# Kernel tuning notes

Hardware: AMD Instinct MI355X
Metric: run time of the kernel (lower is better)

## Reference

```python
import jax, jax.numpy as jnp
import numpy as np

N = 50000      # nodes
E = 800000     # edges
F_IN = 128     # input_channels
H = 128        # hidden_channels
OUT = 10       # output_channels
G = 64         # graphs in batch


def setup_inputs() -> dict:
    key = jax.random.key(0)
    ks = jax.random.split(key, 16)
    s = 0.05
    inp = {
        "x": jax.random.normal(ks[0], (N, F_IN), jnp.float32),
        "edge_index": jax.random.randint(ks[1], (2, E), 0, N, jnp.int64 if jax.config.jax_enable_x64 else jnp.int32),
        "batch": jnp.sort(jax.random.randint(ks[2], (N,), 0, G, jnp.int32)),
        "conv1_w": jax.random.normal(ks[3], (F_IN, H), jnp.float32) * s,
        "conv1_b": jnp.zeros((H,), jnp.float32),
        "conv2_w": jax.random.normal(ks[4], (H, H), jnp.float32) * s,
        "conv2_b": jnp.zeros((H,), jnp.float32),
        "conv3_w": jax.random.normal(ks[5], (H, H), jnp.float32) * s,
        "conv3_b": jnp.zeros((H,), jnp.float32),
        "fc1_w": jax.random.normal(ks[6], (H, 8 * H), jnp.float32) * s,
        "fc1_b": jnp.zeros((8 * H,), jnp.float32),
        "fc2_w": jax.random.normal(ks[7], (8 * H, 4 * H), jnp.float32) * s,
        "fc2_b": jnp.zeros((4 * H,), jnp.float32),
        "fc3_w": jax.random.normal(ks[8], (4 * H, 2 * H), jnp.float32) * s,
        "fc3_b": jnp.zeros((2 * H,), jnp.float32),
        "fc4_w": jax.random.normal(ks[9], (2 * H, H), jnp.float32) * s,
        "fc4_b": jnp.zeros((H,), jnp.float32),
        "fc5_w": jax.random.normal(ks[10], (H, OUT), jnp.float32) * s,
        "fc5_b": jnp.zeros((OUT,), jnp.float32),
    }
    return inp


def _gcn_conv(x, w, b, src, dst, norm, n_nodes):
    # GCNConv: out = D^{-1/2} (A + I) D^{-1/2} X W + b   (self-loops already in src/dst)
    xw = x @ w                                        # [N, H]
    msg = xw[src] * norm[:, None]                     # gather + scale, [E+N, H]
    return jax.ops.segment_sum(msg, dst, num_segments=n_nodes) + b


def reference(x, edge_index, batch,
              conv1_w, conv1_b, conv2_w, conv2_b, conv3_w, conv3_b,
              fc1_w, fc1_b, fc2_w, fc2_b, fc3_w, fc3_b,
              fc4_w, fc4_b, fc5_w, fc5_b):
    n = x.shape[0]
    loop = jnp.arange(n, dtype=edge_index.dtype)
    src = jnp.concatenate([edge_index[0], loop])      # add self-loops
    dst = jnp.concatenate([edge_index[1], loop])
    deg = jax.ops.segment_sum(jnp.ones_like(dst, dtype=x.dtype), dst, num_segments=n)
    dinv = jnp.where(deg > 0, jax.lax.rsqrt(deg), 0.0)
    norm = dinv[src] * dinv[dst]                      # symmetric normalization per edge

    h = jax.nn.relu(_gcn_conv(x, conv1_w, conv1_b, src, dst, norm, n))
    h = jax.nn.relu(_gcn_conv(h, conv2_w, conv2_b, src, dst, norm, n))
    h = _gcn_conv(h, conv3_w, conv3_b, src, dst, norm, n)

    # global mean pool over graphs
    sums = jax.ops.segment_sum(h, batch, num_segments=G)
    cnt = jax.ops.segment_sum(jnp.ones((n,), x.dtype), batch, num_segments=G)
    f = sums / jnp.maximum(cnt, 1.0)[:, None]         # [G, H]

    y = jax.nn.relu(f @ fc1_w + fc1_b)
    y = jax.nn.relu(y @ fc2_w + fc2_b)
    y = jax.nn.relu(y @ fc3_w + fc3_b)
    y = jax.nn.relu(y @ fc4_w + fc4_b)
    # dropout p=0.5 is identity in eval mode
    y = y @ fc5_w + fc5_b                             # [G, OUT]
    return (f, y)
```

## Files before the change

### kernel.cpp

```cpp
#include <hip/hip_runtime.h>
#include <stdint.h>

#define N_NODES 50000
#define N_EDGES 800000
#define FEAT    128
#define NGRAPH  64

#define E_BLKS    3125
#define GEMM_BLKS 6250
#define GR_BLKS   (GEMM_BLKS + E_BLKS)

typedef __attribute__((ext_vector_type(8))) short short8;
typedef __attribute__((ext_vector_type(4))) float floatx4;

static __device__ __forceinline__ ushort f2bf(float f) {
  uint32_t x = __float_as_uint(f);
  x += 0x7FFF + ((x >> 16) & 1);
  return (ushort)(x >> 16);
}
static __device__ __forceinline__ float bfLo(uint32_t u) {
  return __uint_as_float(u << 16);
}
static __device__ __forceinline__ float bfHi(uint32_t u) {
  return __uint_as_float(u & 0xFFFF0000u);
}

static __device__ __forceinline__ void cvt4T(const float* __restrict__ in,
                                             ushort* __restrict__ outT, int i) {
  float4 v = ((const float4*)in)[i];
  int k = (4 * i) >> 7;
  int n = (4 * i) & 127;
  outT[(size_t)(n + 0) * FEAT + k] = f2bf(v.x);
  outT[(size_t)(n + 1) * FEAT + k] = f2bf(v.y);
  outT[(size_t)(n + 2) * FEAT + k] = f2bf(v.z);
  outT[(size_t)(n + 3) * FEAT + k] = f2bf(v.w);
}

__global__ __launch_bounds__(256) void wcvt(const float* __restrict__ w0,
                                            const float* __restrict__ w1,
                                            ushort* __restrict__ wbT) {
  int i = blockIdx.x * 256 + threadIdx.x;
  if (i < 4096) cvt4T(w0, wbT, i);
  else cvt4T(w1, wbT + FEAT * FEAT, i - 4096);
}

static __device__ __forceinline__ void gemm_body_f32a(int wave, int lane,
                                                      const float* __restrict__ X,
                                                      const ushort* __restrict__ WT,
                                                      ushort* __restrict__ XW) {
  int mt = wave >> 3;
  int nt = wave & 7;
  int m0 = mt * 16, n0 = nt * 16;
  int r = lane & 15, quad = lane >> 4;
  floatx4 acc = {0.f, 0.f, 0.f, 0.f};
  const float* xrow = X + (size_t)(m0 + r) * FEAT;
  const ushort* wrow = WT + (size_t)(n0 + r) * FEAT;
#pragma unroll
  for (int kb = 0; kb < 4; ++kb) {
    int k0 = kb * 32 + quad * 8;
    float4 f0 = *(const float4*)(xrow + k0);
    float4 f1 = *(const float4*)(xrow + k0 + 4);
    short8 a;
    a[0] = (short)f2bf(f0.x); a[1] = (short)f2bf(f0.y);
    a[2] = (short)f2bf(f0.z); a[3] = (short)f2bf(f0.w);
    a[4] = (short)f2bf(f1.x); a[5] = (short)f2bf(f1.y);
    a[6] = (short)f2bf(f1.z); a[7] = (short)f2bf(f1.w);
    short8 b = *(const short8*)(wrow + k0);
    acc = __builtin_amdgcn_mfma_f32_16x16x32_bf16(a, b, acc, 0, 0, 0);
  }
#pragma unroll
  for (int reg = 0; reg < 4; ++reg) {
    int row = quad * 4 + reg;
    XW[(size_t)(m0 + row) * FEAT + n0 + r] = f2bf(acc[reg]);
  }
}

__global__ __launch_bounds__(256) void gemm_rank(const float* __restrict__ x,
                                                 const ushort* __restrict__ wbT,
                                                 ushort* __restrict__ msl,
                                                 const int* __restrict__ dst,
                                                 int* __restrict__ cnt,
                                                 int* __restrict__ rank) {
  int b = blockIdx.x, t = threadIdx.x;
  int third = b / 3;
  int rem = b - third * 3;
  if (rem < 2) {
    int gb = third * 2 + rem;
    gemm_body_f32a(gb * 4 + (t >> 6), t & 63, x, wbT, msl);
  } else {
    int e = third * 256 + t;
    rank[e] = atomicAdd(&cnt[dst[e]], 1);
  }
}

__global__ __launch_bounds__(256) void dinv_scan1(const int* __restrict__ cnt,
                                                  const int* __restrict__ batch,
                                                  float* __restrict__ dinv,
                                                  float* __restrict__ cnt_g,
                                                  int* __restrict__ ptr,
                                                  int* __restrict__ bsums) {
  __shared__ int tmp[256];
  __shared__ int bins[NGRAPH];
  if (threadIdx.x < NGRAPH) bins[threadIdx.x] = 0;
  int i = blockIdx.x * 256 + threadIdx.x;
  int v = (i < N_NODES) ? cnt[i] : 0;
  tmp[threadIdx.x] = v;
  __syncthreads();
  for (int off = 1; off < 256; off <<= 1) {
    int t = (threadIdx.x >= off) ? tmp[threadIdx.x - off] : 0;
    __syncthreads();
    tmp[threadIdx.x] += t;
    __syncthreads();
  }
  if (i < N_NODES) ptr[i] = tmp[threadIdx.x] - v;
  if (threadIdx.x == 255) bsums[blockIdx.x] = tmp[255];
  if (i < N_NODES) {
    dinv[i] = rsqrtf((float)v + 1.0f);
    atomicAdd(&bins[batch[i]], 1);
  }
  __syncthreads();
  if (threadIdx.x < NGRAPH && bins[threadIdx.x] > 0)
    atomicAdd(&cnt_g[threadIdx.x], (float)bins[threadIdx.x]);
}

__global__ __launch_bounds__(256) void scan2(int* __restrict__ bsums, int nb) {
  __shared__ int tmp[256];
  int v = (threadIdx.x < nb) ? bsums[threadIdx.x] : 0;
  tmp[threadIdx.x] = v;
  __syncthreads();
  for (int off = 1; off < 256; off <<= 1) {
    int t = (threadIdx.x >= off) ? tmp[threadIdx.x - off] : 0;
    __syncthreads();
    tmp[threadIdx.x] += t;
    __syncthreads();
  }
  if (threadIdx.x < nb) bsums[threadIdx.x] = tmp[threadIdx.x] - v;
}

__global__ __launch_bounds__(256) void scan3(int* __restrict__ ptr,
                                             const int* __restrict__ bsums) {
  int i = blockIdx.x * 256 + threadIdx.x;
  if (i < N_NODES) ptr[i] += bsums[blockIdx.x];
}

__global__ __launch_bounds__(256) void fill_csr(const int* __restrict__ src,
                                                const int* __restrict__ dst,
                                                const int* __restrict__ rank,
                                                const int* __restrict__ ptr,
                                                const float* __restrict__ dinv,
                                                int2* __restrict__ edges) {
  int e = blockIdx.x * 256 + threadIdx.x;
  if (e >= N_EDGES) return;
  int s = src[e];
  edges[ptr[dst[e]] + rank[e]] = make_int2(s, __float_as_int(dinv[s]));
}

__global__ __launch_bounds__(256) void gemm128(const ushort* __restrict__ X,
                                               const ushort* __restrict__ WT,
                                               ushort* __restrict__ XW) {
  int wave = (blockIdx.x * 256 + threadIdx.x) >> 6;
  int lane = threadIdx.x & 63;
  int mt = wave >> 3;
  int nt = wave & 7;
  int m0 = mt * 16, n0 = nt * 16;
  int r = lane & 15, quad = lane >> 4;
  floatx4 acc = {0.f, 0.f, 0.f, 0.f};
  const ushort* xrow = X + (size_t)(m0 + r) * FEAT;
  const ushort* wrow = WT + (size_t)(n0 + r) * FEAT;
#pragma unroll
  for (int kb = 0; kb < 4; ++kb) {
    int k0 = kb * 32 + quad * 8;
    short8 a = *(const short8*)(xrow + k0);
    short8 b = *(const short8*)(wrow + k0);
    acc = __builtin_amdgcn_mfma_f32_16x16x32_bf16(a, b, acc, 0, 0, 0);
  }
#pragma unroll
  for (int reg = 0; reg < 4; ++reg) {
    int row = quad * 4 + reg;
    XW[(size_t)(m0 + row) * FEAT + n0 + r] = f2bf(acc[reg]);
  }
}

template <int MODE>
__global__ __launch_bounds__(256) void agg_kernel(const ushort* __restrict__ msg,
                                                  const float* __restrict__ dinv,
                                                  const int* __restrict__ ptr,
                                                  const int* __restrict__ cnt,
                                                  const int2* __restrict__ edges,
                                                  const float* __restrict__ bias,
                                                  void* __restrict__ outp) {
  int wave = (blockIdx.x * 256 + threadIdx.x) >> 6;
  int lane = threadIdx.x & 63;
  if (wave >= N_NODES) return;
  int v = wave;
  float di = dinv[v];
  const uint32_t* m32 = (const uint32_t*)msg;
  uint32_t su = m32[(size_t)v * 64 + lane];
  float ax0 = di * bfLo(su), ay0 = di * bfHi(su);
  float ax1 = 0.f, ay1 = 0.f, ax2 = 0.f, ay2 = 0.f, ax3 = 0.f, ay3 = 0.f;
  int start = ptr[v];
  int n = cnt[v];
  int i = 0;
  if ((start & 1) && n > 0) {
    int2 e = edges[start];
    uint32_t u = m32[(size_t)e.x * 64 + lane];
    float nrm = __int_as_float(e.y);
    ax0 = fmaf(nrm, bfLo(u), ax0);
    ay0 = fmaf(nrm, bfHi(u), ay0);
    i = 1;
  }
  for (; i + 8 <= n; i += 8) {
    const int4* ep = (const int4*)(edges + start + i);
    int4 q0 = ep[0], q1 = ep[1], q2 = ep[2], q3 = ep[3];
    uint32_t u0 = m32[(size_t)q0.x * 64 + lane];
    uint32_t u1 = m32[(size_t)q0.z * 64 + lane];
    uint32_t u2 = m32[(size_t)q1.x * 64 + lane];
    uint32_t u3 = m32[(size_t)q1.z * 64 + lane];
    uint32_t u4 = m32[(size_t)q2.x * 64 + lane];
    uint32_t u5 = m32[(size_t)q2.z * 64 + lane];
    uint32_t u6 = m32[(size_t)q3.x * 64 + lane];
    uint32_t u7 = m32[(size_t)q3.z * 64 + lane];
    float n0 = __int_as_float(q0.y), n1 = __int_as_float(q0.w);
    float n2 = __int_as_float(q1.y), n3 = __int_as_float(q1.w);
    float n4 = __int_as_float(q2.y), n5 = __int_as_float(q2.w);
    float n6 = __int_as_float(q3.y), n7 = __int_as_float(q3.w);
    ax0 = fmaf(n0, bfLo(u0), ax0); ay0 = fmaf(n0, bfHi(u0), ay0);
    ax1 = fmaf(n1, bfLo(u1), ax1); ay1 = fmaf(n1, bfHi(u1), ay1);
    ax2 = fmaf(n2, bfLo(u2), ax2); ay2 = fmaf(n2, bfHi(u2), ay2);
    ax3 = fmaf(n3, bfLo(u3), ax3); ay3 = fmaf(n3, bfHi(u3), ay3);
    ax0 = fmaf(n4, bfLo(u4), ax0); ay0 = fmaf(n4, bfHi(u4), ay0);
    ax1 = fmaf(n5, bfLo(u5), ax1); ay1 = fmaf(n5, bfHi(u5), ay1);
    ax2 = fmaf(n6, bfLo(u6), ax2); ay2 = fmaf(n6, bfHi(u6), ay2);
    ax3 = fmaf(n7, bfLo(u7), ax3); ay3 = fmaf(n7, bfHi(u7), ay3);
  }
  for (; i < n; ++i) {
    int2 e = edges[start + i];
    float nrm = __int_as_float(e.y);
    uint32_t u = m32[(size_t)e.x * 64 + lane];
    ax0 = fmaf(nrm, bfLo(u), ax0);
    ay0 = fmaf(nrm, bfHi(u), ay0);
  }
  float ax = (ax0 + ax1) + (ax2 + ax3);
  float ay = (ay0 + ay1) + (ay2 + ay3);
  if (MODE == 2) {
    ((float2*)outp)[(size_t)v * 64 + lane] = make_float2(ax * di, ay * di);
  } else {
    ax = fmaf(ax, di, bias[2 * lane]);
    ay = fmaf(ay, di, bias[2 * lane + 1]);
    ax = fmaxf(ax, 0.f);
    ay = fmaxf(ay, 0.f);
    ushort2 h2;
    h2.x = f2bf(ax);
    h2.y = f2bf(ay);
    ((ushort2*)outp)[(size_t)v * 64 + lane] = h2;
  }
}

__global__ __launch_bounds__(256) void pool_sum(const float* __restrict__ a3,
                                                const int* __restrict__ batch,
                                                float* __restrict__ P) {
  int wave = blockIdx.x * 4 + (threadIdx.x >> 6);
  int lane = threadIdx.x & 63;
  int v0 = wave * 16;
  if (v0 >= N_NODES) return;
  int vend = v0 + 16;
  if (vend > N_NODES) vend = N_NODES;
  const float2* a2 = (const float2*)a3;
  float ax = 0.f, ay = 0.f;
  int g = batch[v0];
  for (int v = v0; v < vend; ++v) {
    int gv = batch[v];
    if (gv != g) {
      atomicAdd(&P[(size_t)g * FEAT + 2 * lane], ax);
      atomicAdd(&P[(size_t)g * FEAT + 2 * lane + 1], ay);
      ax = 0.f; ay = 0.f; g = gv;
    }
    float2 t = a2[(size_t)v * 64 + lane];
    ax += t.x;
    ay += t.y;
  }
  atomicAdd(&P[(size_t)g * FEAT + 2 * lane], ax);
  atomicAdd(&P[(size_t)g * FEAT + 2 * lane + 1], ay);
}

template <int K, int C, int KSLICE, int RELU_IN, int DIVC, int NSPLIT>
__global__ __launch_bounds__(256) void fc_layer(const float* __restrict__ IN,
                                                const float* __restrict__ W,
                                                const float* __restrict__ Bs,
                                                const float* __restrict__ cntg,
                                                float* __restrict__ OUT) {
  constexpr int CB = (C + 63) / 64;
  int lane = threadIdx.x & 63;
  int gq = threadIdx.x >> 6;
  int bid = blockIdx.x;
  int kp = bid % NSPLIT;
  int rest = bid / NSPLIT;
  int cg = rest % CB;
  int g = (rest / CB) * 4 + gq;
  int c = cg * 64 + lane;
  if (c >= C) return;
  int k0 = kp * KSLICE;
  const float* wp = W + (size_t)k0 * C + c;
  const float* in = IN + (size_t)g * K + k0;
  float cf = 1.f;
  if (DIVC) cf = fmaxf(cntg[g], 1.f);
  float a0 = 0.f, a1 = 0.f, a2 = 0.f, a3 = 0.f;
  float a4 = 0.f, a5 = 0.f, a6 = 0.f, a7 = 0.f;
#pragma unroll 2
  for (int k = 0; k < KSLICE; k += 8) {
    float i0 = in[k + 0], i1 = in[k + 1], i2 = in[k + 2], i3 = in[k + 3];
    float i4 = in[k + 4], i5 = in[k + 5], i6 = in[k + 6], i7 = in[k + 7];
    if (RELU_IN) {
      i0 = fmaxf(i0, 0.f); i1 = fmaxf(i1, 0.f);
      i2 = fmaxf(i2, 0.f); i3 = fmaxf(i3, 0.f);
      i4 = fmaxf(i4, 0.f); i5 = fmaxf(i5, 0.f);
      i6 = fmaxf(i6, 0.f); i7 = fmaxf(i7, 0.f);
    }
    if (DIVC) {
      i0 /= cf; i1 /= cf; i2 /= cf; i3 /= cf;
      i4 /= cf; i5 /= cf; i6 /= cf; i7 /= cf;
    }
    a0 = fmaf(i0, wp[(size_t)(k + 0) * C], a0);
    a1 = fmaf(i1, wp[(size_t)(k + 1) * C], a1);
    a2 = fmaf(i2, wp[(size_t)(k + 2) * C], a2);
    a3 = fmaf(i3, wp[(size_t)(k + 3) * C], a3);
    a4 = fmaf(i4, wp[(size_t)(k + 4) * C], a4);
    a5 = fmaf(i5, wp[(size_t)(k + 5) * C], a5);
    a6 = fmaf(i6, wp[(size_t)(k + 6) * C], a6);
    a7 = fmaf(i7, wp[(size_t)(k + 7) * C], a7);
  }
  float s = ((a0 + a1) + (a2 + a3)) + ((a4 + a5) + (a6 + a7));
  if (NSPLIT == 1) {
    OUT[(size_t)g * C + c] = s + Bs[c];
  } else {
    atomicAdd(&OUT[(size_t)g * C + c], s + (kp == 0 ? Bs[c] : 0.f));
  }
}

extern "C" void kernel_launch(void* const* d_in, const int* in_sizes, int n_in,
                              void* d_out, int out_size, void* d_ws, size_t ws_size,
                              hipStream_t stream) {
  const float* x         = (const float*)d_in[0];
  const int*   ei        = (const int*)d_in[1];
  const int*   batch     = (const int*)d_in[2];
  const float* conv_w[3] = {(const float*)d_in[3], (const float*)d_in[5], (const float*)d_in[7]};
  const float* conv_b[3] = {(const float*)d_in[4], (const float*)d_in[6], (const float*)d_in[8]};
  const float* fc_w[5]   = {(const float*)d_in[9],  (const float*)d_in[11],
                            (const float*)d_in[13], (const float*)d_in[15],
                            (const float*)d_in[17]};
  const float* fc_b[5]   = {(const float*)d_in[10], (const float*)d_in[12],
                            (const float*)d_in[14], (const float*)d_in[16],
                            (const float*)d_in[18]};
  const int* e_src = ei;
  const int* e_dst = ei + N_EDGES;
  float* out_f = (float*)d_out;
  float* out_y = (float*)d_out + NGRAPH * FEAT;

  char* p = (char*)d_ws;
  auto carve = [&](size_t bytes) {
    char* r = p;
    p += (bytes + 255) & ~(size_t)255;
    return r;
  };
  int*    cnt_i   = (int*)carve(N_NODES * 4);
  float*  dinv    = (float*)carve(N_NODES * 4);
  int*    csr_ptr = (int*)carve(N_NODES * 4);
  int*    bsums   = (int*)carve(256 * 4);
  int2*   edges   = (int2*)carve((size_t)N_EDGES * 8);
  ushort* wbT     = (ushort*)carve((size_t)2 * FEAT * FEAT * 2);
  ushort* hbuf    = (ushort*)carve((size_t)N_NODES * FEAT * 2);
  float*  f_sum   = (float*)carve(NGRAPH * FEAT * 4);
  float*  cnt_g   = (float*)carve(NGRAPH * 4);
  float*  Y1      = (float*)carve(NGRAPH * 1024 * 4);
  float*  Y2      = (float*)carve(NGRAPH * 512 * 4);
  float*  Y3      = (float*)carve(NGRAPH * 256 * 4);
  float*  Y4      = (float*)carve(NGRAPH * 128 * 4);
  char*   region  = carve((size_t)N_NODES * FEAT * 4);
  int*    rank    = (int*)region;
  ushort* msl     = (ushort*)(region + (size_t)N_EDGES * 4);
  float*  a3      = (float*)region;

  const int BLK_N = (N_NODES + 255) / 256;

  hipMemsetAsync(cnt_i, 0, N_NODES * 4, stream);
  hipMemsetAsync(f_sum, 0, NGRAPH * FEAT * 4 + 256, stream);
  hipMemsetAsync(Y2, 0, NGRAPH * (512 + 256 + 128) * 4, stream);

  wcvt<<<32, 256, 0, stream>>>(conv_w[0], conv_w[1], wbT);

  gemm_rank<<<GR_BLKS, 256, 0, stream>>>(x, wbT, msl, e_dst, cnt_i, rank);

  dinv_scan1<<<BLK_N, 256, 0, stream>>>(cnt_i, batch, dinv, cnt_g, csr_ptr, bsums);
  scan2<<<1, 256, 0, stream>>>(bsums, BLK_N);
  scan3<<<BLK_N, 256, 0, stream>>>(csr_ptr, bsums);

  fill_csr<<<E_BLKS, 256, 0, stream>>>(e_src, e_dst, rank, csr_ptr, dinv, edges);

  const int AGG_BLKS  = (N_NODES + 3) / 4;
  const int POOL_BLKS = (N_NODES / 16 + 3) / 4 + 1;

  agg_kernel<0><<<AGG_BLKS, 256, 0, stream>>>(msl, dinv, csr_ptr, cnt_i, edges,
                                              conv_b[0], hbuf);
  gemm128<<<GEMM_BLKS, 256, 0, stream>>>(hbuf, wbT + FEAT * FEAT, msl);
  agg_kernel<0><<<AGG_BLKS, 256, 0, stream>>>(msl, dinv, csr_ptr, cnt_i, edges,
                                              conv_b[1], hbuf);
  agg_kernel<2><<<AGG_BLKS, 256, 0, stream>>>(hbuf, dinv, csr_ptr, cnt_i, edges,
                                              nullptr, a3);
  pool_sum<<<POOL_BLKS, 256, 0, stream>>>(a3, batch, f_sum);

  fc_layer< 128, 128, 128, 0, 1, 1><<< 32, 256, 0, stream>>>(f_sum, conv_w[2], conv_b[2], cnt_g, out_f);
  fc_layer< 128,1024, 128, 0, 0, 1><<<256, 256, 0, stream>>>(out_f, fc_w[0], fc_b[0], nullptr, Y1);
  fc_layer<1024, 512, 256, 1, 0, 4><<<512, 256, 0, stream>>>(Y1, fc_w[1], fc_b[1], nullptr, Y2);
  fc_layer< 512, 256, 128, 1, 0, 4><<<256, 256, 0, stream>>>(Y2, fc_w[2], fc_b[2], nullptr, Y3);
  fc_layer< 256, 128,  32, 1, 0, 8><<<256, 256, 0, stream>>>(Y3, fc_w[3], fc_b[3], nullptr, Y4);
  fc_layer< 128,  10, 128, 1, 0, 1><<< 16, 256, 0, stream>>>(Y4, fc_w[4], fc_b[4], nullptr, out_y);
}
```

Measured before the change: 375.0 us.

## Fuse layer-1 aggregation with layer-2 GEMM and use row-strip GEMM

Layer-1 aggregation now writes its ReLU'd bf16 features for 16 nodes into shared memory, and the same block runs the layer-2 MFMA GEMM on them. This removes the separate gemm128 launch and the round trip of the hidden buffer through global memory. The first GEMM in gemm_rank also changes so each wave computes a full 16-row strip across all 8 column tiles, converting X rows once instead of eight times. This shifts the block ratio with the rank atomics to 1:4. The fused kernel uses 512-thread blocks and a block-wide barrier, which may lower occupancy for the gather-heavy aggregation phase.

```diff
diff --git a/kernel.cpp b/kernel.cpp
--- a/kernel.cpp
+++ b/kernel.cpp
@@ -6,9 +6,9 @@
 #define FEAT    128
 #define NGRAPH  64
 
-#define E_BLKS    3125
-#define GEMM_BLKS 6250
-#define GR_BLKS   (GEMM_BLKS + E_BLKS)
+#define E_BLKS      3125
+#define GSTRIP_BLKS 782
+#define GR_BLKS     (GSTRIP_BLKS + E_BLKS)
 
 typedef __attribute__((ext_vector_type(8))) short short8;
 typedef __attribute__((ext_vector_type(4))) float floatx4;
@@ -44,17 +44,15 @@
   else cvt4T(w1, wbT + FEAT * FEAT, i - 4096);
 }
 
-static __device__ __forceinline__ void gemm_body_f32a(int wave, int lane,
-                                                      const float* __restrict__ X,
-                                                      const ushort* __restrict__ WT,
-                                                      ushort* __restrict__ XW) {
-  int mt = wave >> 3;
-  int nt = wave & 7;
-  int m0 = mt * 16, n0 = nt * 16;
+static __device__ __forceinline__ void gemm_strip_f32a(int strip, int lane,
+                                                       const float* __restrict__ X,
+                                                       const ushort* __restrict__ WT,
+                                                       ushort* __restrict__ XW) {
+  if (strip >= N_NODES / 16) return;
+  int m0 = strip * 16;
   int r = lane & 15, quad = lane >> 4;
-  floatx4 acc = {0.f, 0.f, 0.f, 0.f};
   const float* xrow = X + (size_t)(m0 + r) * FEAT;
-  const ushort* wrow = WT + (size_t)(n0 + r) * FEAT;
+  short8 afr[4];
 #pragma unroll
   for (int kb = 0; kb < 4; ++kb) {
     int k0 = kb * 32 + quad * 8;
@@ -65,13 +63,21 @@
     a[2] = (short)f2bf(f0.z); a[3] = (short)f2bf(f0.w);
     a[4] = (short)f2bf(f1.x); a[5] = (short)f2bf(f1.y);
     a[6] = (short)f2bf(f1.z); a[7] = (short)f2bf(f1.w);
-    short8 b = *(const short8*)(wrow + k0);
-    acc = __builtin_amdgcn_mfma_f32_16x16x32_bf16(a, b, acc, 0, 0, 0);
-  }
-#pragma unroll
-  for (int reg = 0; reg < 4; ++reg) {
-    int row = quad * 4 + reg;
-    XW[(size_t)(m0 + row) * FEAT + n0 + r] = f2bf(acc[reg]);
+    afr[kb] = a;
+  }
+#pragma unroll
+  for (int nt = 0; nt < 8; ++nt) {
+    int n0 = nt * 16;
+    floatx4 acc = {0.f, 0.f, 0.f, 0.f};
+    const ushort* wrow = WT + (size_t)(n0 + r) * FEAT;
+#pragma unroll
+    for (int kb = 0; kb < 4; ++kb) {
+      short8 b = *(const short8*)(wrow + kb * 32 + quad * 8);
+      acc = __builtin_amdgcn_mfma_f32_16x16x32_bf16(afr[kb], b, acc, 0, 0, 0);
+    }
+#pragma unroll
+    for (int reg = 0; reg < 4; ++reg)
+      XW[(size_t)(m0 + quad * 4 + reg) * FEAT + n0 + r] = f2bf(acc[reg]);
   }
 }
 
@@ -82,13 +88,11 @@
                                                  int* __restrict__ cnt,
                                                  int* __restrict__ rank) {
   int b = blockIdx.x, t = threadIdx.x;
-  int third = b / 3;
-  int rem = b - third * 3;
-  if (rem < 2) {
-    int gb = third * 2 + rem;
-    gemm_body_f32a(gb * 4 + (t >> 6), t & 63, x, wbT, msl);
+  int fifth = b / 5;
+  if (b - fifth * 5 == 0) {
+    gemm_strip_f32a(fifth * 4 + (t >> 6), t & 63, x, wbT, msl);
   } else {
-    int e = third * 256 + t;
+    int e = (b - fifth - 1) * 256 + t;
     rank[e] = atomicAdd(&cnt[dst[e]], 1);
   }
 }
@@ -155,51 +159,11 @@
   edges[ptr[dst[e]] + rank[e]] = make_int2(s, __float_as_int(dinv[s]));
 }
 
-__global__ __launch_bounds__(256) void gemm128(const ushort* __restrict__ X,
-                                               const ushort* __restrict__ WT,
-                                               ushort* __restrict__ XW) {
-  int wave = (blockIdx.x * 256 + threadIdx.x) >> 6;
-  int lane = threadIdx.x & 63;
-  int mt = wave >> 3;
-  int nt = wave & 7;
-  int m0 = mt * 16, n0 = nt * 16;
-  int r = lane & 15, quad = lane >> 4;
-  floatx4 acc = {0.f, 0.f, 0.f, 0.f};
-  const ushort* xrow = X + (size_t)(m0 + r) * FEAT;
-  const ushort* wrow = WT + (size_t)(n0 + r) * FEAT;
-#pragma unroll
-  for (int kb = 0; kb < 4; ++kb) {
-    int k0 = kb * 32 + quad * 8;
-    short8 a = *(const short8*)(xrow + k0);
-    short8 b = *(const short8*)(wrow + k0);
-    acc = __builtin_amdgcn_mfma_f32_16x16x32_bf16(a, b, acc, 0, 0, 0);
-  }
-#pragma unroll
-  for (int reg = 0; reg < 4; ++reg) {
-    int row = quad * 4 + reg;
-    XW[(size_t)(m0 + row) * FEAT + n0 + r] = f2bf(acc[reg]);
-  }
-}
-
-template <int MODE>
-__global__ __launch_bounds__(256) void agg_kernel(const ushort* __restrict__ msg,
-                                                  const float* __restrict__ dinv,
-                                                  const int* __restrict__ ptr,
-                                                  const int* __restrict__ cnt,
+static __device__ __forceinline__ float2 agg_node(const uint32_t* __restrict__ m32,
                                                   const int2* __restrict__ edges,
-                                                  const float* __restrict__ bias,
-                                                  void* __restrict__ outp) {
-  int wave = (blockIdx.x * 256 + threadIdx.x) >> 6;
-  int lane = threadIdx.x & 63;
-  if (wave >= N_NODES) return;
-  int v = wave;
-  float di = dinv[v];
-  const uint32_t* m32 = (const uint32_t*)msg;
-  uint32_t su = m32[(size_t)v * 64 + lane];
-  float ax0 = di * bfLo(su), ay0 = di * bfHi(su);
-  float ax1 = 0.f, ay1 = 0.f, ax2 = 0.f, ay2 = 0.f, ax3 = 0.f, ay3 = 0.f;
-  int start = ptr[v];
-  int n = cnt[v];
+                                                  int start, int n, int lane) {
+  float ax0 = 0.f, ay0 = 0.f, ax1 = 0.f, ay1 = 0.f;
+  float ax2 = 0.f, ay2 = 0.f, ax3 = 0.f, ay3 = 0.f;
   int i = 0;
   if ((start & 1) && n > 0) {
     int2 e = edges[start];
@@ -240,18 +204,79 @@
     ax0 = fmaf(nrm, bfLo(u), ax0);
     ay0 = fmaf(nrm, bfHi(u), ay0);
   }
-  float ax = (ax0 + ax1) + (ax2 + ax3);
-  float ay = (ay0 + ay1) + (ay2 + ay3);
+  return make_float2((ax0 + ax1) + (ax2 + ax3), (ay0 + ay1) + (ay2 + ay3));
+}
+
+__global__ __launch_bounds__(512) void agg1_gemm2(const ushort* __restrict__ msg,
+                                                  const float* __restrict__ dinv,
+                                                  const int* __restrict__ ptr,
+                                                  const int* __restrict__ cnt,
+                                                  const int2* __restrict__ edges,
+                                                  const float* __restrict__ bias,
+                                                  const ushort* __restrict__ wT2,
+                                                  ushort* __restrict__ msl2) {
+  __shared__ ushort h1s[16][136];
+  int w = threadIdx.x >> 6, lane = threadIdx.x & 63;
+  int base = blockIdx.x * 16;
+  const uint32_t* m32 = (const uint32_t*)msg;
+  float blo = bias[2 * lane], bhi = bias[2 * lane + 1];
+#pragma unroll
+  for (int vi = 0; vi < 2; ++vi) {
+    int li = w * 2 + vi;
+    int v = base + li;
+    float di = dinv[v];
+    uint32_t su = m32[(size_t)v * 64 + lane];
+    float2 s = agg_node(m32, edges, ptr[v], cnt[v], lane);
+    float ax = fmaf(fmaf(di, bfLo(su), s.x), di, blo);
+    float ay = fmaf(fmaf(di, bfHi(su), s.y), di, bhi);
+    ushort2 hp;
+    hp.x = f2bf(fmaxf(ax, 0.f));
+    hp.y = f2bf(fmaxf(ay, 0.f));
+    *(ushort2*)&h1s[li][2 * lane] = hp;
+  }
+  __syncthreads();
+  int r = lane & 15, quad = lane >> 4;
+  int n0 = w * 16;
+  floatx4 acc = {0.f, 0.f, 0.f, 0.f};
+  const ushort* wrow = wT2 + (size_t)(n0 + r) * FEAT;
+#pragma unroll
+  for (int kb = 0; kb < 4; ++kb) {
+    int k0 = kb * 32 + quad * 8;
+    short8 a = *(const short8*)&h1s[r][k0];
+    short8 b = *(const short8*)(wrow + k0);
+    acc = __builtin_amdgcn_mfma_f32_16x16x32_bf16(a, b, acc, 0, 0, 0);
+  }
+#pragma unroll
+  for (int reg = 0; reg < 4; ++reg)
+    msl2[(size_t)(base + quad * 4 + reg) * FEAT + n0 + r] = f2bf(acc[reg]);
+}
+
+template <int MODE>
+__global__ __launch_bounds__(256) void agg_kernel(const ushort* __restrict__ msg,
+                                                  const float* __restrict__ dinv,
+                                                  const int* __restrict__ ptr,
+                                                  const int* __restrict__ cnt,
+                                                  const int2* __restrict__ edges,
+                                                  const float* __restrict__ bias,
+                                                  void* __restrict__ outp) {
+  int wave = (blockIdx.x * 256 + threadIdx.x) >> 6;
+  int lane = threadIdx.x & 63;
+  if (wave >= N_NODES) return;
+  int v = wave;
+  float di = dinv[v];
+  const uint32_t* m32 = (const uint32_t*)msg;
+  uint32_t su = m32[(size_t)v * 64 + lane];
+  float2 s = agg_node(m32, edges, ptr[v], cnt[v], lane);
+  float ax = fmaf(di, bfLo(su), s.x);
+  float ay = fmaf(di, bfHi(su), s.y);
   if (MODE == 2) {
     ((float2*)outp)[(size_t)v * 64 + lane] = make_float2(ax * di, ay * di);
   } else {
     ax = fmaf(ax, di, bias[2 * lane]);
     ay = fmaf(ay, di, bias[2 * lane + 1]);
-    ax = fmaxf(ax, 0.f);
-    ay = fmaxf(ay, 0.f);
     ushort2 h2;
-    h2.x = f2bf(ax);
-    h2.y = f2bf(ay);
+    h2.x = f2bf(fmaxf(ax, 0.f));
+    h2.y = f2bf(fmaxf(ay, 0.f));
     ((ushort2*)outp)[(size_t)v * 64 + lane] = h2;
   }
 }
@@ -368,16 +393,17 @@
   int*    bsums   = (int*)carve(256 * 4);
   int2*   edges   = (int2*)carve((size_t)N_EDGES * 8);
   ushort* wbT     = (ushort*)carve((size_t)2 * FEAT * FEAT * 2);
-  ushort* hbuf    = (ushort*)carve((size_t)N_NODES * FEAT * 2);
+  ushort* h2buf   = (ushort*)carve((size_t)N_NODES * FEAT * 2);
   float*  f_sum   = (float*)carve(NGRAPH * FEAT * 4);
   float*  cnt_g   = (float*)carve(NGRAPH * 4);
   float*  Y1      = (float*)carve(NGRAPH * 1024 * 4);
   float*  Y2      = (float*)carve(NGRAPH * 512 * 4);
   float*  Y3      = (float*)carve(NGRAPH * 256 * 4);
   float*  Y4      = (float*)carve(NGRAPH * 128 * 4);
-  char*   region  = carve((size_t)N_NODES * FEAT * 4);
+  char*   region  = carve((size_t)N_EDGES * 4 + 2 * (size_t)N_NODES * FEAT * 2);
   int*    rank    = (int*)region;
-  ushort* msl     = (ushort*)(region + (size_t)N_EDGES * 4);
+  ushort* msl1    = (ushort*)(region + (size_t)N_EDGES * 4);
+  ushort* msl2    = (ushort*)(region + (size_t)N_EDGES * 4 + (size_t)N_NODES * FEAT * 2);
   float*  a3      = (float*)region;
 
   const int BLK_N = (N_NODES + 255) / 256;
@@ -388,7 +414,7 @@
 
   wcvt<<<32, 256, 0, stream>>>(conv_w[0], conv_w[1], wbT);
 
-  gemm_rank<<<GR_BLKS, 256, 0, stream>>>(x, wbT, msl, e_dst, cnt_i, rank);
+  gemm_rank<<<GR_BLKS, 256, 0, stream>>>(x, wbT, msl1, e_dst, cnt_i, rank);
 
   dinv_scan1<<<BLK_N, 256, 0, stream>>>(cnt_i, batch, dinv, cnt_g, csr_ptr, bsums);
   scan2<<<1, 256, 0, stream>>>(bsums, BLK_N);
@@ -399,12 +425,11 @@
   const int AGG_BLKS  = (N_NODES + 3) / 4;
   const int POOL_BLKS = (N_NODES / 16 + 3) / 4 + 1;
 
-  agg_kernel<0><<<AGG_BLKS, 256, 0, stream>>>(msl, dinv, csr_ptr, cnt_i, edges,
-                                              conv_b[0], hbuf);
-  gemm128<<<GEMM_BLKS, 256, 0, stream>>>(hbuf, wbT + FEAT * FEAT, msl);
-  agg_kernel<0><<<AGG_BLKS, 256, 0, stream>>>(msl, dinv, csr_ptr, cnt_i, edges,
-                                              conv_b[1], hbuf);
-  agg_kernel<2><<<AGG_BLKS, 256, 0, stream>>>(hbuf, dinv, csr_ptr, cnt_i, edges,
+  agg1_gemm2<<<N_NODES / 16, 512, 0, stream>>>(msl1, dinv, csr_ptr, cnt_i, edges,
+                                               conv_b[0], wbT + FEAT * FEAT, msl2);
+  agg_kernel<0><<<AGG_BLKS, 256, 0, stream>>>(msl2, dinv, csr_ptr, cnt_i, edges,
+                                              conv_b[1], h2buf);
+  agg_kernel<2><<<AGG_BLKS, 256, 0, stream>>>(h2buf, dinv, csr_ptr, cnt_i, edges,
                                               nullptr, a3);
   pool_sum<<<POOL_BLKS, 256, 0, stream>>>(a3, batch, f_sum);
 
```

Measured after the change: 374.0 us. No clear change (-0.3%).
